# Performance work log

Hardware: AMD Instinct MI355X
Metric: run time of the kernel (lower is better)

## Reference

```python
import jax, jax.numpy as jnp
import numpy as np
import math

T, B, V, D = 8, 32, 50257, 256
N = 4096            # memory slots
H = 4               # attention heads
L = 2               # transformer layers
K = 3               # shift width
HALF = K // 2
WIN = 16            # controller window
RH, WH = 1, 1       # read / write heads
EPS = 1e-12


def _pe(win, d):
    pos = jnp.arange(win, dtype=jnp.float32)[:, None]
    div = jnp.exp(jnp.arange(0, d, 2, dtype=jnp.float32) * (-math.log(10000.0) / d))
    pe = jnp.zeros((win, d), dtype=jnp.float32)
    pe = pe.at[:, 0::2].set(jnp.sin(pos * div))
    pe = pe.at[:, 1::2].set(jnp.cos(pos * div))
    return pe[:, None, :]


def _ln(x, g, b, eps=1e-5):
    mu = x.mean(-1, keepdims=True)
    var = ((x - mu) ** 2).mean(-1, keepdims=True)
    return (x - mu) * jax.lax.rsqrt(var + eps) * g + b


def _mha(x, Wqkv, bqkv, Wo, bo):
    S, Bc, Dm = x.shape
    dh = Dm // H
    qkv = x @ Wqkv.T + bqkv
    q, k, v = jnp.split(qkv, 3, axis=-1)
    q = q.reshape(S, Bc, H, dh)
    k = k.reshape(S, Bc, H, dh)
    v = v.reshape(S, Bc, H, dh)
    logits = jnp.einsum('sbhd,tbhd->bhst', q, k) / math.sqrt(dh)
    a = jax.nn.softmax(logits, axis=-1)
    o = jnp.einsum('bhst,tbhd->sbhd', a, v).reshape(S, Bc, Dm)
    return o @ Wo.T + bo


def _addressing(key_v, beta, gate, shift, gamma, prev_w, memory):
    # key_v [B,M], beta/gate/gamma [B,1], shift [B,K], prev_w [B,N], memory [B,N,M]
    key_n = key_v / (jnp.linalg.norm(key_v, axis=-1, keepdims=True) + EPS)
    mem_n = memory / (jnp.linalg.norm(memory, axis=-1, keepdims=True) + EPS)
    cos = jnp.einsum('bnm,bm->bn', mem_n, key_n)
    wc = jax.nn.softmax(jax.nn.softplus(beta) * cos, axis=-1)
    g = jax.nn.sigmoid(gate)
    wg = g * wc + (1.0 - g) * prev_w
    s = jax.nn.softmax(shift, axis=-1)
    shifted = sum(s[:, k:k + 1] * jnp.roll(wg, k - HALF, axis=-1) for k in range(K))
    gp = 1.0 + jax.nn.softplus(gamma)
    wt = (shifted + EPS) ** gp
    return wt / (wt.sum(-1, keepdims=True) + EPS)


def setup_inputs() -> dict:
    key = jax.random.key(0)
    ks = iter(jax.random.split(key, 40))
    def w(shape, s=0.02):
        return jax.random.normal(next(ks), shape, jnp.float32) * s
    return {
        'tokens': jax.random.randint(next(ks), (T, B), 0, V, jnp.int32),
        'emb_W': w((V, D)),
        'read_gate_W': w((D, D)), 'read_gate_b': jnp.zeros((D,)),
        'film_W': w((2 * D, D)), 'film_b': jnp.zeros((2 * D,)),
        't_Wqkv': w((L, 3 * D, D)), 't_bqkv': jnp.zeros((L, 3 * D)),
        't_Wo': w((L, D, D)), 't_bo': jnp.zeros((L, D)),
        't_ln1_g': jnp.ones((L, D)), 't_ln1_b': jnp.zeros((L, D)),
        't_ln2_g': jnp.ones((L, D)), 't_ln2_b': jnp.zeros((L, D)),
        't_W1': w((L, 4 * D, D)), 't_b1': jnp.zeros((L, 4 * D)),
        't_W2': w((L, D, 4 * D)), 't_b2': jnp.zeros((L, D)),
        'out_ln_g': jnp.ones((D,)), 'out_ln_b': jnp.zeros((D,)),
        'lstm_Wih': w((2, 4 * D, D)), 'lstm_Whh': w((2, 4 * D, D)),
        'lstm_bih': jnp.zeros((2, 4 * D)), 'lstm_bhh': jnp.zeros((2, 4 * D)),
        'head_W': w((V, D)), 'head_b': jnp.zeros((V,)),
        'read_W': w((D + 3 + K, D)), 'read_b': jnp.zeros((D + 3 + K,)),
        'write_W': w((3 * D + 3 + K, D)), 'write_b': jnp.zeros((3 * D + 3 + K,)),
    }


def reference(tokens, emb_W, read_gate_W, read_gate_b, film_W, film_b,
              t_Wqkv, t_bqkv, t_Wo, t_bo, t_ln1_g, t_ln1_b, t_ln2_g, t_ln2_b,
              t_W1, t_b1, t_W2, t_b2, out_ln_g, out_ln_b,
              lstm_Wih, lstm_Whh, lstm_bih, lstm_bhh,
              head_W, head_b, read_W, read_b, write_W, write_b):
    pe = _pe(WIN, D)
    memory = jnp.zeros((B, N, D), jnp.float32)
    read_w = jnp.zeros((B, RH, N), jnp.float32).at[:, :, 0].set(1.0)
    write_w = jnp.zeros((B, WH, N), jnp.float32).at[:, :, 0].set(1.0)
    record = jnp.zeros((B, D), jnp.float32)
    hx = jnp.zeros((2, B, D), jnp.float32)
    cx = jnp.zeros((2, B, D), jnp.float32)
    hist = jnp.zeros((1, B, D), jnp.float32)
    logits_all = []
    for t in range(T):  # T fixed, sequential recurrence (context length grows)
        emb = emb_W[tokens[t]]                               # [B,D]
        r = jnp.einsum('bhn,bnm->bm', read_w, memory)        # sum over read heads
        fp = record @ film_W.T + film_b
        gam = 1.0 + jnp.tanh(fp[:, :D])
        bet = fp[:, D:]
        rg = jax.nn.sigmoid(record @ read_gate_W.T + read_gate_b)
        x_in = gam * emb + bet + rg * r
        ctx = jnp.concatenate([hist, x_in[None]], axis=0)
        if ctx.shape[0] > WIN:
            ctx = ctx[-WIN:]
        hist = ctx
        h = ctx + pe[:ctx.shape[0]]
        for l in range(L):  # norm_first pre-LN encoder layers (eval, relu FFN)
            h = h + _mha(_ln(h, t_ln1_g[l], t_ln1_b[l]), t_Wqkv[l], t_bqkv[l], t_Wo[l], t_bo[l])
            h = h + (jax.nn.relu(_ln(h, t_ln2_g[l], t_ln2_b[l]) @ t_W1[l].T + t_b1[l]) @ t_W2[l].T + t_b2[l])
        c_out = _ln(h[-1], out_ln_g, out_ln_b)
        # 2-layer LSTM single step (torch gate order i,f,g,o)
        x_l = c_out
        new_h, new_c = [], []
        for l in range(2):
            gates = x_l @ lstm_Wih[l].T + lstm_bih[l] + hx[l] @ lstm_Whh[l].T + lstm_bhh[l]
            i_g, f_g, g_g, o_g = jnp.split(gates, 4, axis=-1)
            c_new = jax.nn.sigmoid(f_g) * cx[l] + jax.nn.sigmoid(i_g) * jnp.tanh(g_g)
            h_new = jax.nn.sigmoid(o_g) * jnp.tanh(c_new)
            new_h.append(h_new); new_c.append(c_new)
            x_l = h_new
        hx = jnp.stack(new_h); cx = jnp.stack(new_c)
        record = hx[-1]
        c_out = c_out + x_l
        logits_all.append(c_out @ head_W.T + head_b)
        # read addressing
        rp = (c_out @ read_W.T + read_b).reshape(B, RH, -1)
        new_rw = []
        for hh in range(RH):
            p = rp[:, hh]
            new_rw.append(_addressing(p[:, :D], p[:, D:D + 1], p[:, D + 1:D + 2],
                                      p[:, D + 2:D + 2 + K], p[:, D + 2 + K:D + 3 + K],
                                      read_w[:, hh], memory))
        read_w = jnp.stack(new_rw, axis=1)
        # write addressing + erase/add (addressing uses pre-update memory)
        wp = (c_out @ write_W.T + write_b).reshape(B, WH, -1)
        mem_pre = memory
        new_ww = []
        for hh in range(WH):
            p = wp[:, hh]
            wt = _addressing(p[:, :D], p[:, D:D + 1], p[:, D + 1:D + 2],
                             p[:, D + 2:D + 2 + K], p[:, D + 2 + K:D + 3 + K],
                             write_w[:, hh], mem_pre)
            erase = jax.nn.sigmoid(p[:, D + 3 + K:2 * D + 3 + K])
            add = jnp.tanh(p[:, 2 * D + 3 + K:3 * D + 3 + K])
            memory = memory * (1.0 - wt[:, :, None] * erase[:, None, :]) + wt[:, :, None] * add[:, None, :]
            new_ww.append(wt)
        write_w = jnp.stack(new_ww, axis=1)
    return jnp.stack(logits_all, axis=0)  # [T, B, V]
```

## Files before the change

### kernel.cpp

```cpp
#include <hip/hip_runtime.h>
#include <math.h>

#define TT 8
#define BB 32
#define VV 50257
#define DD 256
#define NN 4096
#define EPS_ 1e-12f

typedef __attribute__((ext_vector_type(8))) short short8;
typedef __attribute__((ext_vector_type(4))) float f32x4;

__device__ __forceinline__ float sigf(float x) { return 1.f / (1.f + expf(-x)); }
__device__ __forceinline__ float softplusf_(float x) { return fmaxf(x, 0.f) + log1pf(expf(-fabsf(x))); }
__device__ __forceinline__ unsigned f2bf(float f) {
  union { float f; unsigned u; } c; c.f = f;
  return (c.u + 0x7FFFu + ((c.u >> 16) & 1u)) >> 16;
}
__device__ __forceinline__ float bf2f(unsigned u16) {
  union { unsigned u; float f; } c; c.u = u16 << 16; return c.f;
}

__device__ __forceinline__ float blk_sum(float v, float* s) {
#pragma unroll
  for (int o = 32; o > 0; o >>= 1) v += __shfl_down(v, o);
  __syncthreads();
  if ((threadIdx.x & 63) == 0) s[threadIdx.x >> 6] = v;
  __syncthreads();
  return s[0] + s[1] + s[2] + s[3];
}
__device__ __forceinline__ float blk_max(float v, float* s) {
#pragma unroll
  for (int o = 32; o > 0; o >>= 1) v = fmaxf(v, __shfl_down(v, o));
  __syncthreads();
  if ((threadIdx.x & 63) == 0) s[threadIdx.x >> 6] = v;
  __syncthreads();
  return fmaxf(fmaxf(s[0], s[1]), fmaxf(s[2], s[3]));
}

__global__ void init_k(float* rw, float* ww, float* hpe) {
  int i = blockIdx.x * 256 + threadIdx.x;
  if (i < BB) { rw[(size_t)i * NN] = 1.f; ww[(size_t)i * NN] = 1.f; }
  if (i < BB * DD) hpe[i] = (i & 1) ? 1.f : 0.f;
}

__global__ void cvtw_k(const float* __restrict__ W, unsigned short* __restrict__ Wh, int n4) {
  int i = blockIdx.x * 256 + threadIdx.x;
  if (i >= n4) return;
  float4 v = *(const float4*)(W + (size_t)i * 4);
  uint2 p;
  p.x = f2bf(v.x) | (f2bf(v.y) << 16);
  p.y = f2bf(v.z) | (f2bf(v.w) << 16);
  *(uint2*)(Wh + (size_t)i * 4) = p;
}

__global__ void catlstm_k(const float* __restrict__ Wih, const float* __restrict__ Whh,
                          const float* __restrict__ bih, const float* __restrict__ bhh,
                          unsigned short* __restrict__ Wc, float* __restrict__ cb) {
  int i = blockIdx.x * 256 + threadIdx.x;
  if (i >= 2 * 1024 * 512) return;
  int k = i & 511, np = (i >> 9) & 1023, l = i >> 19;
  int d = np >> 2, gate = np & 3;
  int src = gate * 256 + d;
  float v = (k < 256) ? Wih[((size_t)l * 1024 + src) * 256 + k]
                      : Whh[((size_t)l * 1024 + src) * 256 + (k - 256)];
  Wc[i] = (unsigned short)f2bf(v);
  if (k == 0) cb[l * 1024 + np] = bih[l * 1024 + src] + bhh[l * 1024 + src];
}

__global__ void catrw_k(const float* __restrict__ rW, const float* __restrict__ rb,
                        const float* __restrict__ wW, const float* __restrict__ wb,
                        unsigned short* __restrict__ Wrw, float* __restrict__ brw) {
  int i = blockIdx.x * 256 + threadIdx.x;
  if (i >= 1036 * 256) return;
  int k = i & 255, n = i >> 8;
  float v = (n < 262) ? rW[(size_t)n * 256 + k] : wW[(size_t)(n - 262) * 256 + k];
  Wrw[i] = (unsigned short)f2bf(v);
  if (k == 0) brw[n] = (n < 262) ? rb[n] : wb[n - 262];
}

__global__ void brc_k(const float* __restrict__ fb, const float* __restrict__ rb, float* __restrict__ brc) {
  int i = blockIdx.x * 256 + threadIdx.x;
  if (i < 512) brc[i] = fb[i];
  else if (i < 768) brc[i] = rb[i - 512];
}

__global__ __launch_bounds__(256) void ln0_k(const float* __restrict__ hpe,
                                             const float* __restrict__ g1, const float* __restrict__ b1,
                                             unsigned short* __restrict__ q1b) {
  __shared__ float s8[8];
  int b = blockIdx.x, d = threadIdx.x;
  float v = hpe[(size_t)b * 256 + d];
  float mu = blk_sum(v, s8) * (1.f / 256.f);
  float dd = v - mu;
  float var = blk_sum(dd * dd, s8) * (1.f / 256.f);
  float rs = rsqrtf(var + 1e-5f);
  q1b[(size_t)b * 256 + d] = (unsigned short)f2bf(dd * rs * g1[d] + b1[d]);
}

template <int EPI>
__global__ __launch_bounds__(256) void gA_k(const unsigned short* __restrict__ A,
                                            const unsigned short* __restrict__ W,
                                            const float* __restrict__ bias,
                                            float* __restrict__ Cf,
                                            unsigned short* __restrict__ Cb,
                                            int ldc, int Nlim) {
  const int tid = threadIdx.x, w = tid >> 6, l = tid & 63, r = l & 15, q = l >> 4;
  const int m0 = blockIdx.y * 32;
  const int n = blockIdx.x * 64 + w * 16 + r;
  const unsigned short* Ap = A + (size_t)m0 * 256;
  const unsigned short* Wp = W + (size_t)n * 256;
  f32x4 acc0 = {0.f, 0.f, 0.f, 0.f}, acc1 = {0.f, 0.f, 0.f, 0.f};
#pragma unroll
  for (int kt = 0; kt < 8; ++kt) {
    short8 a0 = *(const short8*)(Ap + r * 256 + kt * 32 + q * 8);
    short8 a1 = *(const short8*)(Ap + (16 + r) * 256 + kt * 32 + q * 8);
    short8 bf = *(const short8*)(Wp + kt * 32 + q * 8);
    acc0 = __builtin_amdgcn_mfma_f32_16x16x32_bf16(a0, bf, acc0, 0, 0, 0);
    acc1 = __builtin_amdgcn_mfma_f32_16x16x32_bf16(a1, bf, acc1, 0, 0, 0);
  }
  if (n >= Nlim) return;
  float bb = bias[n];
#pragma unroll
  for (int e = 0; e < 4; ++e) {
    int m1 = m0 + q * 4 + e, m2 = m1 + 16;
    float v1 = acc0[e] + bb, v2 = acc1[e] + bb;
    if constexpr (EPI == 0) {
      Cf[(size_t)m1 * ldc + n] = v1;
      Cf[(size_t)m2 * ldc + n] = v2;
    } else {
      Cb[(size_t)m1 * ldc + n] = (unsigned short)f2bf(fmaxf(v1, 0.f));
      Cb[(size_t)m2 * ldc + n] = (unsigned short)f2bf(fmaxf(v2, 0.f));
    }
  }
}

template <int K, int OLN>
__global__ __launch_bounds__(256) void gB_k(const unsigned short* __restrict__ A,
                                            const unsigned short* __restrict__ W,
                                            const float* __restrict__ bias,
                                            const float* __restrict__ resid,
                                            float* __restrict__ Hout,
                                            const float* __restrict__ lng,
                                            const float* __restrict__ lnb,
                                            unsigned short* __restrict__ Xb, int xstride,
                                            float* __restrict__ c_out) {
  __shared__ float hv[32][260];
  const int tid = threadIdx.x, w = tid >> 6, l = tid & 63, r = l & 15, q = l >> 4;
  const int m0 = blockIdx.x * 32;
  const unsigned short* Ap = A + (size_t)m0 * K;
  const unsigned short* Wp0 = W + (size_t)(w * 64 + 0 + r) * K;
  const unsigned short* Wp1 = W + (size_t)(w * 64 + 16 + r) * K;
  const unsigned short* Wp2 = W + (size_t)(w * 64 + 32 + r) * K;
  const unsigned short* Wp3 = W + (size_t)(w * 64 + 48 + r) * K;
  f32x4 acc0[4], acc1[4];
#pragma unroll
  for (int j = 0; j < 4; ++j) { acc0[j] = {0.f, 0.f, 0.f, 0.f}; acc1[j] = {0.f, 0.f, 0.f, 0.f}; }
#pragma unroll 4
  for (int kt = 0; kt < K / 32; ++kt) {
    short8 a0 = *(const short8*)(Ap + (size_t)r * K + kt * 32 + q * 8);
    short8 a1 = *(const short8*)(Ap + (size_t)(16 + r) * K + kt * 32 + q * 8);
    short8 b0 = *(const short8*)(Wp0 + kt * 32 + q * 8);
    short8 b1 = *(const short8*)(Wp1 + kt * 32 + q * 8);
    short8 b2 = *(const short8*)(Wp2 + kt * 32 + q * 8);
    short8 b3 = *(const short8*)(Wp3 + kt * 32 + q * 8);
    acc0[0] = __builtin_amdgcn_mfma_f32_16x16x32_bf16(a0, b0, acc0[0], 0, 0, 0);
    acc1[0] = __builtin_amdgcn_mfma_f32_16x16x32_bf16(a1, b0, acc1[0], 0, 0, 0);
    acc0[1] = __builtin_amdgcn_mfma_f32_16x16x32_bf16(a0, b1, acc0[1], 0, 0, 0);
    acc1[1] = __builtin_amdgcn_mfma_f32_16x16x32_bf16(a1, b1, acc1[1], 0, 0, 0);
    acc0[2] = __builtin_amdgcn_mfma_f32_16x16x32_bf16(a0, b2, acc0[2], 0, 0, 0);
    acc1[2] = __builtin_amdgcn_mfma_f32_16x16x32_bf16(a1, b2, acc1[2], 0, 0, 0);
    acc0[3] = __builtin_amdgcn_mfma_f32_16x16x32_bf16(a0, b3, acc0[3], 0, 0, 0);
    acc1[3] = __builtin_amdgcn_mfma_f32_16x16x32_bf16(a1, b3, acc1[3], 0, 0, 0);
  }
#pragma unroll
  for (int j = 0; j < 4; ++j) {
    int n = w * 64 + j * 16 + r;
    float bb = bias[n];
#pragma unroll
    for (int e = 0; e < 4; ++e) {
      int m1 = q * 4 + e, m2 = m1 + 16;
      float v1 = acc0[j][e] + bb + resid[(size_t)(m0 + m1) * 256 + n];
      float v2 = acc1[j][e] + bb + resid[(size_t)(m0 + m2) * 256 + n];
      Hout[(size_t)(m0 + m1) * 256 + n] = v1;
      Hout[(size_t)(m0 + m2) * 256 + n] = v2;
      hv[m1][n] = v1;
      hv[m2][n] = v2;
    }
  }
  __syncthreads();
  const float4 g4 = *(const float4*)(lng + l * 4);
  const float4 be4 = *(const float4*)(lnb + l * 4);
#pragma unroll
  for (int i = 0; i < 8; ++i) {
    int row = w * 8 + i;
    float4 v = *(const float4*)&hv[row][l * 4];
    float s1 = v.x + v.y + v.z + v.w;
    float s2 = v.x * v.x + v.y * v.y + v.z * v.z + v.w * v.w;
#pragma unroll
    for (int o = 32; o > 0; o >>= 1) { s1 += __shfl_xor(s1, o); s2 += __shfl_xor(s2, o); }
    float mu = s1 * (1.f / 256.f);
    float var = fmaxf(s2 * (1.f / 256.f) - mu * mu, 0.f);
    float rs = rsqrtf(var + 1e-5f);
    float y0 = (v.x - mu) * rs * g4.x + be4.x;
    float y1 = (v.y - mu) * rs * g4.y + be4.y;
    float y2 = (v.z - mu) * rs * g4.z + be4.z;
    float y3 = (v.w - mu) * rs * g4.w + be4.w;
    uint2 pk;
    pk.x = f2bf(y0) | (f2bf(y1) << 16);
    pk.y = f2bf(y2) | (f2bf(y3) << 16);
    *(uint2*)(Xb + (size_t)(m0 + row) * xstride + l * 4) = pk;
    if constexpr (OLN) {
      float4 cv = make_float4(y0, y1, y2, y3);
      *(float4*)(c_out + (size_t)(m0 + row) * 256 + l * 4) = cv;
    }
  }
}

template <int LAST>
__global__ __launch_bounds__(256) void gL_k(const unsigned short* __restrict__ A,
                                            const unsigned short* __restrict__ W,
                                            const float* __restrict__ cbias,
                                            float* __restrict__ cx,
                                            unsigned short* __restrict__ li_own,
                                            unsigned short* __restrict__ li_next,
                                            const float* __restrict__ c_outp,
                                            unsigned short* __restrict__ cfinb,
                                            unsigned short* __restrict__ record_b) {
  __shared__ float g[32][68];
  const int tid = threadIdx.x, w = tid >> 6, l = tid & 63, r = l & 15, q = l >> 4;
  const int n = blockIdx.x * 64 + w * 16 + r;
  const unsigned short* Wp = W + (size_t)n * 512;
  f32x4 acc0 = {0.f, 0.f, 0.f, 0.f}, acc1 = {0.f, 0.f, 0.f, 0.f};
#pragma unroll 4
  for (int kt = 0; kt < 16; ++kt) {
    short8 a0 = *(const short8*)(A + (size_t)r * 512 + kt * 32 + q * 8);
    short8 a1 = *(const short8*)(A + (size_t)(16 + r) * 512 + kt * 32 + q * 8);
    short8 bf = *(const short8*)(Wp + kt * 32 + q * 8);
    acc0 = __builtin_amdgcn_mfma_f32_16x16x32_bf16(a0, bf, acc0, 0, 0, 0);
    acc1 = __builtin_amdgcn_mfma_f32_16x16x32_bf16(a1, bf, acc1, 0, 0, 0);
  }
  float bb = cbias[n];
  int nb = w * 16 + r;
#pragma unroll
  for (int e = 0; e < 4; ++e) {
    g[q * 4 + e][nb] = acc0[e] + bb;
    g[16 + q * 4 + e][nb] = acc1[e] + bb;
  }
  __syncthreads();
#pragma unroll
  for (int h2 = 0; h2 < 2; ++h2) {
    int u = tid + 256 * h2;
    int b = u >> 4, dd = u & 15;
    int dg = blockIdx.x * 16 + dd;
    float gi = g[b][dd * 4 + 0], gf = g[b][dd * 4 + 1];
    float gg = g[b][dd * 4 + 2], go = g[b][dd * 4 + 3];
    float c = sigf(gf) * cx[b * 256 + dg] + sigf(gi) * tanhf(gg);
    float hN = sigf(go) * tanhf(c);
    cx[b * 256 + dg] = c;
    li_own[(size_t)b * 512 + 256 + dg] = (unsigned short)f2bf(hN);
    if constexpr (LAST) {
      record_b[b * 256 + dg] = (unsigned short)f2bf(hN);
      cfinb[b * 256 + dg] = (unsigned short)f2bf(c_outp[b * 256 + dg] + hN);
    } else {
      li_next[(size_t)b * 512 + dg] = (unsigned short)f2bf(hN);
    }
  }
}

__global__ __launch_bounds__(256) void xinpw_k(const int* __restrict__ tokens,
                                               const float* __restrict__ embW,
                                               const float* __restrict__ fp,
                                               const float* __restrict__ rvec,
                                               const float* __restrict__ g1, const float* __restrict__ b1,
                                               float* __restrict__ hpe,
                                               unsigned short* __restrict__ q1b, int t) {
  __shared__ float s8[8];
  int b = blockIdx.x, d = threadIdx.x;
  float gam = 1.f + tanhf(fp[(size_t)b * 768 + d]);
  float bet = fp[(size_t)b * 768 + 256 + d];
  float rg = sigf(fp[(size_t)b * 768 + 512 + d]);
  int tok = tokens[t * BB + b];
  float emb = embW[(size_t)tok * 256 + d];
  float ang = (float)(t + 1) * expf(-logf(10000.f) * (float)(d & ~1) / 256.f);
  float pe = (d & 1) ? cosf(ang) : sinf(ang);
  float x = gam * emb + bet + rg * rvec[b * 256 + d] + pe;
  hpe[((size_t)(t + 1) * BB + b) * 256 + d] = x;
  float mu = blk_sum(x, s8) * (1.f / 256.f);
  float dd = x - mu;
  float var = blk_sum(dd * dd, s8) * (1.f / 256.f);
  float rs = rsqrtf(var + 1e-5f);
  q1b[((size_t)(t + 1) * BB + b) * 256 + d] = (unsigned short)f2bf(dd * rs * g1[d] + b1[d]);
}

__global__ __launch_bounds__(128) void attn_k(const float* __restrict__ qkv,
                                              unsigned short* __restrict__ ao, int S) {
  int bh = blockIdx.x;
  int b = bh >> 2, h = bh & 3;
  __shared__ float q[9][64], k[9][64], v[9][64], lg[9][12];
  int tid = threadIdx.x;
  for (int i = tid; i < S * 64; i += 128) {
    int s = i >> 6, d = i & 63;
    const float* base = qkv + (size_t)(s * BB + b) * 768 + h * 64 + d;
    q[s][d] = base[0]; k[s][d] = base[256]; v[s][d] = base[512];
  }
  __syncthreads();
  for (int p = tid; p < S * S; p += 128) {
    int s = p / S, t2 = p % S;
    float acc = 0.f;
    for (int d = 0; d < 64; ++d) acc += q[s][d] * k[t2][d];
    lg[s][t2] = acc * 0.125f;
  }
  __syncthreads();
  if (tid < S) {
    float mx = -1e30f;
    for (int t2 = 0; t2 < S; ++t2) mx = fmaxf(mx, lg[tid][t2]);
    float sum = 0.f;
    for (int t2 = 0; t2 < S; ++t2) { float e = expf(lg[tid][t2] - mx); lg[tid][t2] = e; sum += e; }
    float inv = 1.f / sum;
    for (int t2 = 0; t2 < S; ++t2) lg[tid][t2] *= inv;
  }
  __syncthreads();
  for (int i = tid; i < S * 64; i += 128) {
    int s = i >> 6, d = i & 63;
    float o = 0.f;
    for (int t2 = 0; t2 < S; ++t2) o += lg[s][t2] * v[t2][d];
    ao[(size_t)(s * BB + b) * 256 + h * 64 + d] = (unsigned short)f2bf(o);
  }
}

__global__ __launch_bounds__(64) void attnl_k(const float* __restrict__ qkv,
                                              unsigned short* __restrict__ ao, int S) {
  int bh = blockIdx.x;
  int b = bh >> 2, h = bh & 3;
  int d = threadIdx.x;
  __shared__ float sc[9];
  float qd = qkv[(size_t)((S - 1) * BB + b) * 768 + h * 64 + d];
  for (int j = 0; j < S; ++j) {
    float p = qd * qkv[(size_t)(j * BB + b) * 768 + h * 64 + 256 + d];
#pragma unroll
    for (int o = 32; o > 0; o >>= 1) p += __shfl_down(p, o);
    if (d == 0) sc[j] = p * 0.125f;
  }
  __syncthreads();
  float mx = -1e30f;
  for (int j = 0; j < S; ++j) mx = fmaxf(mx, sc[j]);
  float pj[9], sum = 0.f;
  for (int j = 0; j < S; ++j) { pj[j] = expf(sc[j] - mx); sum += pj[j]; }
  float inv = 1.f / sum;
  float o = 0.f;
  for (int j = 0; j < S; ++j) o += pj[j] * inv * qkv[(size_t)(j * BB + b) * 768 + h * 64 + 512 + d];
  ao[(size_t)b * 256 + h * 64 + d] = (unsigned short)f2bf(o);
}

__global__ __launch_bounds__(256) void head_k(const unsigned short* __restrict__ Wh,
                                              const unsigned short* __restrict__ Ah,
                                              const float* __restrict__ hb,
                                              float* __restrict__ out) {
  const int tid = threadIdx.x;
  const int w = tid >> 6, l = tid & 63;
  const int r = l & 15, q = l >> 4;
  const int n = blockIdx.x * 64 + w * 16 + r;
  const int nc = n < VV ? n : VV - 1;
  const short* Ap = (const short*)Ah;
  const short* Wp = (const short*)Wh + (size_t)nc * 256;
  short8 a0[8], a1[8], bf[8];
#pragma unroll
  for (int kt = 0; kt < 8; ++kt) {
    a0[kt] = *(const short8*)(Ap + r * 256 + kt * 32 + q * 8);
    a1[kt] = *(const short8*)(Ap + (16 + r) * 256 + kt * 32 + q * 8);
    bf[kt] = *(const short8*)(Wp + kt * 32 + q * 8);
  }
  f32x4 acc0 = {0.f, 0.f, 0.f, 0.f}, acc1 = {0.f, 0.f, 0.f, 0.f};
#pragma unroll
  for (int kt = 0; kt < 8; ++kt) {
    acc0 = __builtin_amdgcn_mfma_f32_16x16x32_bf16(a0[kt], bf[kt], acc0, 0, 0, 0);
    acc1 = __builtin_amdgcn_mfma_f32_16x16x32_bf16(a1[kt], bf[kt], acc1, 0, 0, 0);
  }
  if (n < VV) {
    float bb = hb[n];
#pragma unroll
    for (int e = 0; e < 4; ++e) {
      int m = q * 4 + e;
      out[(size_t)m * VV + n] = acc0[e] + bb;
      out[(size_t)(16 + m) * VV + n] = acc1[e] + bb;
    }
  }
}

__global__ __launch_bounds__(256) void passA_k(const unsigned short* __restrict__ mem,
                                               const float* __restrict__ rpwp,
                                               float* __restrict__ dr,
                                               float* __restrict__ dw,
                                               float* __restrict__ nrm) {
  __shared__ float kr[256], kw[256];
  int b = blockIdx.y, tid = threadIdx.x;
  kr[tid] = rpwp[(size_t)b * 1036 + tid];
  kw[tid] = rpwp[(size_t)b * 1036 + 262 + tid];
  __syncthreads();
  int w = tid >> 6, lane = tid & 63;
  float4 kr4 = *(float4*)&kr[lane * 4];
  float4 kw4 = *(float4*)&kw[lane * 4];
  int n0 = blockIdx.x * 16 + w * 4;
  for (int rr = 0; rr < 4; ++rr) {
    int n = n0 + rr;
    const unsigned short* row = mem + ((size_t)b * NN + n) * 256;
    uint2 p = *(const uint2*)(row + lane * 4);
    float m0 = bf2f(p.x & 0xffffu), m1 = bf2f(p.x >> 16);
    float m2 = bf2f(p.y & 0xffffu), m3 = bf2f(p.y >> 16);
    float pr = m0 * kr4.x + m1 * kr4.y + m2 * kr4.z + m3 * kr4.w;
    float pw = m0 * kw4.x + m1 * kw4.y + m2 * kw4.z + m3 * kw4.w;
    float pn = m0 * m0 + m1 * m1 + m2 * m2 + m3 * m3;
#pragma unroll
    for (int o = 32; o > 0; o >>= 1) {
      pr += __shfl_down(pr, o); pw += __shfl_down(pw, o); pn += __shfl_down(pn, o);
    }
    if (lane == 0) {
      dr[(size_t)b * NN + n] = pr;
      dw[(size_t)b * NN + n] = pw;
      nrm[(size_t)b * NN + n] = pn;
    }
  }
}

__global__ __launch_bounds__(256) void addr_k(const float* __restrict__ dr,
                                              const float* __restrict__ dw,
                                              const float* __restrict__ nrm,
                                              const float* __restrict__ rpwp,
                                              float* rw, float* ww,
                                              float* __restrict__ ea,
                                              float* __restrict__ rvec) {
  __shared__ float wg[4096];
  __shared__ float s8[8];
  int head = blockIdx.x & 1, b = blockIdx.x >> 1;
  int tid = threadIdx.x;
  const float* p = rpwp + (size_t)b * 1036 + (head ? 262 : 0);
  const float* dot = (head ? dw : dr) + (size_t)b * NN;
  const float* n2 = nrm + (size_t)b * NN;
  float* wout = (head ? ww : rw) + (size_t)b * NN;

  float kv = p[tid];
  float kn = sqrtf(blk_sum(kv * kv, s8)) + EPS_;
  float beta = p[256], gate = p[257], sh0 = p[258], sh1 = p[259], sh2 = p[260], gamma = p[261];
  float spb = softplusf_(beta);
  float g = sigf(gate);
  float mx3 = fmaxf(sh0, fmaxf(sh1, sh2));
  float e0 = expf(sh0 - mx3), e1 = expf(sh1 - mx3), e2 = expf(sh2 - mx3);
  float esum = e0 + e1 + e2;
  float s0 = e0 / esum, s1 = e1 / esum, s2 = e2 / esum;
  float gp = 1.f + softplusf_(gamma);

  float l[16];
  float lmax = -1e30f;
#pragma unroll
  for (int i = 0; i < 16; ++i) {
    int n = tid + i * 256;
    float cs = dot[n] / ((sqrtf(n2[n]) + EPS_) * kn);
    l[i] = spb * cs;
    lmax = fmaxf(lmax, l[i]);
  }
  float Mx = blk_max(lmax, s8);
  float es = 0.f;
#pragma unroll
  for (int i = 0; i < 16; ++i) { l[i] = expf(l[i] - Mx); es += l[i]; }
  float SS = blk_sum(es, s8);
  float inv = 1.f / SS;
#pragma unroll
  for (int i = 0; i < 16; ++i) {
    int n = tid + i * 256;
    wg[n] = g * l[i] * inv + (1.f - g) * wout[n];
  }
  __syncthreads();
  float wt[16];
  float wsum = 0.f;
#pragma unroll
  for (int i = 0; i < 16; ++i) {
    int n = tid + i * 256;
    float sh = s0 * wg[(n + 1) & 4095] + s1 * wg[n] + s2 * wg[(n + 4095) & 4095];
    wt[i] = powf(sh + EPS_, gp);
    wsum += wt[i];
  }
  float WS = blk_sum(wsum, s8) + EPS_;
  float winv = 1.f / WS;
#pragma unroll
  for (int i = 0; i < 16; ++i) wout[tid + i * 256] = wt[i] * winv;

  if (head) {
    ea[(size_t)b * 512 + tid] = sigf(p[262 + tid]);
    ea[(size_t)b * 512 + 256 + tid] = tanhf(p[518 + tid]);
  } else {
    rvec[(size_t)b * 256 + tid] = 0.f;
  }
}

template <int FIRST>
__global__ __launch_bounds__(256) void passB_k(unsigned short* mem, const float* __restrict__ ww,
                                               const float* __restrict__ rw,
                                               const float* __restrict__ ea,
                                               float* __restrict__ rvec) {
  __shared__ float eS[256], aS[256];
  __shared__ float rred[4][256];
  int b = blockIdx.y, tid = threadIdx.x;
  eS[tid] = ea[(size_t)b * 512 + tid];
  aS[tid] = ea[(size_t)b * 512 + 256 + tid];
  __syncthreads();
  int w = tid >> 6, lane = tid & 63;
  float4 e4 = *(float4*)&eS[lane * 4];
  float4 a4 = *(float4*)&aS[lane * 4];
  float4 racc = make_float4(0.f, 0.f, 0.f, 0.f);
  int n0 = blockIdx.x * 128 + w * 32;
  for (int rr = 0; rr < 32; ++rr) {
    int n = n0 + rr;
    float wt = ww[(size_t)b * NN + n];
    float rwv = rw[(size_t)b * NN + n];
    unsigned short* row = mem + ((size_t)b * NN + n) * 256;
    float m0, m1, m2, m3;
    if (FIRST) {
      m0 = wt * a4.x; m1 = wt * a4.y; m2 = wt * a4.z; m3 = wt * a4.w;
    } else {
      uint2 p = *(const uint2*)(row + lane * 4);
      m0 = bf2f(p.x & 0xffffu) * (1.f - wt * e4.x) + wt * a4.x;
      m1 = bf2f(p.x >> 16) * (1.f - wt * e4.y) + wt * a4.y;
      m2 = bf2f(p.y & 0xffffu) * (1.f - wt * e4.z) + wt * a4.z;
      m3 = bf2f(p.y >> 16) * (1.f - wt * e4.w) + wt * a4.w;
    }
    uint2 pk;
    pk.x = f2bf(m0) | (f2bf(m1) << 16);
    pk.y = f2bf(m2) | (f2bf(m3) << 16);
    *(uint2*)(row + lane * 4) = pk;
    racc.x += rwv * m0; racc.y += rwv * m1; racc.z += rwv * m2; racc.w += rwv * m3;
  }
  rred[w][lane * 4 + 0] = racc.x;
  rred[w][lane * 4 + 1] = racc.y;
  rred[w][lane * 4 + 2] = racc.z;
  rred[w][lane * 4 + 3] = racc.w;
  __syncthreads();
  float s = rred[0][tid] + rred[1][tid] + rred[2][tid] + rred[3][tid];
  atomicAdd(rvec + (size_t)b * 256 + tid, s);
}

extern "C" void kernel_launch(void* const* d_in, const int* in_sizes, int n_in,
                              void* d_out, int out_size, void* d_ws, size_t ws_size,
                              hipStream_t stream) {
  const int* tokens = (const int*)d_in[0];
  const float* emb_W = (const float*)d_in[1];
  const float* read_gate_W = (const float*)d_in[2];
  const float* read_gate_b = (const float*)d_in[3];
  const float* film_W = (const float*)d_in[4];
  const float* film_b = (const float*)d_in[5];
  const float* t_Wqkv = (const float*)d_in[6];
  const float* t_bqkv = (const float*)d_in[7];
  const float* t_Wo = (const float*)d_in[8];
  const float* t_bo = (const float*)d_in[9];
  const float* t_ln1_g = (const float*)d_in[10];
  const float* t_ln1_b = (const float*)d_in[11];
  const float* t_ln2_g = (const float*)d_in[12];
  const float* t_ln2_b = (const float*)d_in[13];
  const float* t_W1 = (const float*)d_in[14];
  const float* t_b1 = (const float*)d_in[15];
  const float* t_W2 = (const float*)d_in[16];
  const float* t_b2 = (const float*)d_in[17];
  const float* out_ln_g = (const float*)d_in[18];
  const float* out_ln_b = (const float*)d_in[19];
  const float* lstm_Wih = (const float*)d_in[20];
  const float* lstm_Whh = (const float*)d_in[21];
  const float* lstm_bih = (const float*)d_in[22];
  const float* lstm_bhh = (const float*)d_in[23];
  const float* head_W = (const float*)d_in[24];
  const float* head_b = (const float*)d_in[25];
  const float* read_W = (const float*)d_in[26];
  const float* read_b = (const float*)d_in[27];
  const float* write_W = (const float*)d_in[28];
  const float* write_b = (const float*)d_in[29];
  float* out = (float*)d_out;

  float* ws = (float*)d_ws;
  size_t off = 0;
  float* read_w = ws + off; off += (size_t)BB * NN;
  float* write_w = ws + off; off += (size_t)BB * NN;
  float* cx = ws + off; off += 2 * BB * DD;
  float* r_vec = ws + off; off += BB * DD;
  float* dot_r = ws + off; off += (size_t)BB * NN;
  float* dot_w = ws + off; off += (size_t)BB * NN;
  float* norm2 = ws + off; off += (size_t)BB * NN;
  unsigned short* record_b = (unsigned short*)(ws + off); off += BB * DD / 2;
  unsigned short* lstm_in_b = (unsigned short*)(ws + off); off += 2 * BB * 512 / 2;
  size_t zero_floats = off;
  unsigned short* memory = (unsigned short*)(ws + off); off += (size_t)BB * NN * DD / 2;
  float* hpe = ws + off; off += 9 * BB * DD;
  float* h = ws + off; off += 9 * BB * DD;
  float* h2 = ws + off; off += BB * DD;
  float* qkvC = ws + off; off += 9 * BB * 768;
  float* qkv2 = ws + off; off += 9 * BB * 768;
  float* fp = ws + off; off += BB * 768;
  float* c_out = ws + off; off += BB * DD;
  float* rpwp = ws + off; off += BB * 1036;
  float* ea = ws + off; off += BB * 2 * DD;
  unsigned short* q1b = (unsigned short*)(ws + off); off += 9 * BB * DD / 2;
  unsigned short* q2b = (unsigned short*)(ws + off); off += 9 * BB * DD / 2;
  unsigned short* x2b = (unsigned short*)(ws + off); off += 9 * BB * DD / 2;
  unsigned short* x2b2 = (unsigned short*)(ws + off); off += BB * DD / 2;
  unsigned short* ao_b = (unsigned short*)(ws + off); off += 9 * BB * DD / 2;
  unsigned short* ao2_b = (unsigned short*)(ws + off); off += BB * DD / 2;
  unsigned short* mid_b = (unsigned short*)(ws + off); off += 9 * BB * 1024 / 2;
  unsigned short* cfinb = (unsigned short*)(ws + off); off += BB * DD / 2;
  unsigned short* Wh = (unsigned short*)(ws + off); off += (size_t)VV * 256 / 2;
  unsigned short* Wq_b = (unsigned short*)(ws + off); off += 2 * 768 * 256 / 2;
  unsigned short* Wo_b = (unsigned short*)(ws + off); off += 2 * 256 * 256 / 2;
  unsigned short* W1_b = (unsigned short*)(ws + off); off += 2 * 1024 * 256 / 2;
  unsigned short* W2_b = (unsigned short*)(ws + off); off += 2 * 256 * 1024 / 2;
  unsigned short* Wc_b = (unsigned short*)(ws + off); off += 2 * 1024 * 512 / 2;
  unsigned short* Wrw_b = (unsigned short*)(ws + off); off += 1088 * 256 / 2;
  unsigned short* FR_b = (unsigned short*)(ws + off); off += 768 * 256 / 2;
  float* cb2 = ws + off; off += 2 * 1024;
  float* brw = ws + off; off += 1040;
  float* brc = ws + off; off += 768;
  if (ws_size < off * sizeof(float)) return;

  (void)hipMemsetAsync(ws, 0, zero_floats * sizeof(float), stream);
  (void)hipMemsetAsync(Wrw_b + (size_t)1036 * 256, 0, (size_t)52 * 256 * 2, stream);
  init_k<<<32, 256, 0, stream>>>(read_w, write_w, hpe);
  cvtw_k<<<(VV * 256 / 4 + 255) / 256, 256, 0, stream>>>(head_W, Wh, VV * 256 / 4);
  cvtw_k<<<(2 * 768 * 256 / 4 + 255) / 256, 256, 0, stream>>>(t_Wqkv, Wq_b, 2 * 768 * 256 / 4);
  cvtw_k<<<(2 * 256 * 256 / 4 + 255) / 256, 256, 0, stream>>>(t_Wo, Wo_b, 2 * 256 * 256 / 4);
  cvtw_k<<<(2 * 1024 * 256 / 4 + 255) / 256, 256, 0, stream>>>(t_W1, W1_b, 2 * 1024 * 256 / 4);
  cvtw_k<<<(2 * 256 * 1024 / 4 + 255) / 256, 256, 0, stream>>>(t_W2, W2_b, 2 * 256 * 1024 / 4);
  cvtw_k<<<(512 * 256 / 4 + 255) / 256, 256, 0, stream>>>(film_W, FR_b, 512 * 256 / 4);
  cvtw_k<<<(256 * 256 / 4 + 255) / 256, 256, 0, stream>>>(read_gate_W, FR_b + 512 * 256, 256 * 256 / 4);
  catlstm_k<<<4096, 256, 0, stream>>>(lstm_Wih, lstm_Whh, lstm_bih, lstm_bhh, Wc_b, cb2);
  catrw_k<<<1036, 256, 0, stream>>>(read_W, read_b, write_W, write_b, Wrw_b, brw);
  brc_k<<<3, 256, 0, stream>>>(film_b, read_gate_b, brc);
  ln0_k<<<BB, 256, 0, stream>>>(hpe, t_ln1_g, t_ln1_b, q1b);
  gA_k<0><<<dim3(12, 1), 256, 0, stream>>>(q1b, Wq_b, t_bqkv, qkvC, nullptr, 768, 768);

  for (int t = 0; t < TT; ++t) {
    const int S = t + 2;

    gA_k<0><<<dim3(12, 1), 256, 0, stream>>>(record_b, FR_b, brc, fp, nullptr, 768, 768);
    xinpw_k<<<BB, 256, 0, stream>>>(tokens, emb_W, fp, r_vec, t_ln1_g, t_ln1_b, hpe, q1b, t);
    gA_k<0><<<dim3(12, 1), 256, 0, stream>>>(q1b + (size_t)(t + 1) * BB * 256, Wq_b, t_bqkv,
                                             qkvC + (size_t)(t + 1) * BB * 768, nullptr, 768, 768);
    attn_k<<<BB * 4, 128, 0, stream>>>(qkvC, ao_b, S);
    gB_k<256, 0><<<S, 256, 0, stream>>>(ao_b, Wo_b, t_bo, hpe, h, t_ln2_g, t_ln2_b, x2b, 256, nullptr);
    gA_k<1><<<dim3(16, S), 256, 0, stream>>>(x2b, W1_b, t_b1, nullptr, mid_b, 1024, 1024);
    gB_k<1024, 0><<<S, 256, 0, stream>>>(mid_b, W2_b, t_b2, h, h, t_ln1_g + 256, t_ln1_b + 256, q2b, 256, nullptr);

    gA_k<0><<<dim3(12, S), 256, 0, stream>>>(q2b, Wq_b + 768 * 256, t_bqkv + 768, qkv2, nullptr, 768, 768);
    attnl_k<<<BB * 4, 64, 0, stream>>>(qkv2, ao2_b, S);
    gB_k<256, 0><<<1, 256, 0, stream>>>(ao2_b, Wo_b + 256 * 256, t_bo + 256, h + (size_t)(S - 1) * BB * 256,
                                        h2, t_ln2_g + 256, t_ln2_b + 256, x2b2, 256, nullptr);
    gA_k<1><<<dim3(16, 1), 256, 0, stream>>>(x2b2, W1_b + 1024 * 256, t_b1 + 1024, nullptr, mid_b, 1024, 1024);
    gB_k<1024, 1><<<1, 256, 0, stream>>>(mid_b, W2_b + 256 * 1024, t_b2 + 256, h2, h2,
                                         out_ln_g, out_ln_b, lstm_in_b, 512, c_out);

    gL_k<0><<<16, 256, 0, stream>>>(lstm_in_b, Wc_b, cb2, cx, lstm_in_b, lstm_in_b + BB * 512,
                                    nullptr, nullptr, nullptr);
    gL_k<1><<<16, 256, 0, stream>>>(lstm_in_b + BB * 512, Wc_b + (size_t)1024 * 512, cb2 + 1024,
                                    cx + BB * DD, lstm_in_b + BB * 512, nullptr, c_out, cfinb, record_b);

    head_k<<<(VV + 63) / 64, 256, 0, stream>>>(Wh, cfinb, head_b, out + (size_t)t * BB * VV);

    if (t < TT - 1) {
      gA_k<0><<<dim3(17, 1), 256, 0, stream>>>(cfinb, Wrw_b, brw, rpwp, nullptr, 1036, 1036);
      if (t > 0)
        passA_k<<<dim3(NN / 16, BB), 256, 0, stream>>>(memory, rpwp, dot_r, dot_w, norm2);
      addr_k<<<2 * BB, 256, 0, stream>>>(dot_r, dot_w, norm2, rpwp, read_w, write_w, ea, r_vec);
      if (t == 0)
        passB_k<1><<<dim3(NN / 128, BB), 256, 0, stream>>>(memory, write_w, read_w, ea, r_vec);
      else
        passB_k<0><<<dim3(NN / 128, BB), 256, 0, stream>>>(memory, write_w, read_w, ea, r_vec);
    }
  }
}
```

Before: 1.679 ms.

## Fuse per-step controller kernels into persistent kernel with grid barrier

```diff
diff --git a/kernel.cpp b/kernel.cpp
--- a/kernel.cpp
+++ b/kernel.cpp
@@ -6,6 +6,7 @@
 #define VV 50257
 #define DD 256
 #define NN 4096
+#define NB 144
 #define EPS_ 1e-12f
 
 typedef __attribute__((ext_vector_type(8))) short short8;
@@ -36,6 +37,24 @@
   if ((threadIdx.x & 63) == 0) s[threadIdx.x >> 6] = v;
   __syncthreads();
   return fmaxf(fmaxf(s[0], s[1]), fmaxf(s[2], s[3]));
+}
+
+__device__ __forceinline__ void gbar(unsigned* cnt, unsigned* gen) {
+  __syncthreads();
+  if (threadIdx.x == 0) {
+    __threadfence();
+    unsigned g = __hip_atomic_load(gen, __ATOMIC_RELAXED, __HIP_MEMORY_SCOPE_AGENT);
+    unsigned a = __hip_atomic_fetch_add(cnt, 1u, __ATOMIC_ACQ_REL, __HIP_MEMORY_SCOPE_AGENT);
+    if (a == NB - 1) {
+      __hip_atomic_store(cnt, 0u, __ATOMIC_RELAXED, __HIP_MEMORY_SCOPE_AGENT);
+      __hip_atomic_fetch_add(gen, 1u, __ATOMIC_RELEASE, __HIP_MEMORY_SCOPE_AGENT);
+    } else {
+      while (__hip_atomic_load(gen, __ATOMIC_ACQUIRE, __HIP_MEMORY_SCOPE_AGENT) == g)
+        __builtin_amdgcn_s_sleep(2);
+    }
+    __threadfence();
+  }
+  __syncthreads();
 }
 
 __global__ void init_k(float* rw, float* ww, float* hpe) {
@@ -98,23 +117,18 @@
   q1b[(size_t)b * 256 + d] = (unsigned short)f2bf(dd * rs * g1[d] + b1[d]);
 }
 
-template <int EPI>
-__global__ __launch_bounds__(256) void gA_k(const unsigned short* __restrict__ A,
-                                            const unsigned short* __restrict__ W,
-                                            const float* __restrict__ bias,
-                                            float* __restrict__ Cf,
-                                            unsigned short* __restrict__ Cb,
-                                            int ldc, int Nlim) {
+__device__ __forceinline__ void gA32f_dev(const unsigned short* __restrict__ A,
+                                          const unsigned short* __restrict__ W,
+                                          const float* __restrict__ bias,
+                                          float* __restrict__ Cf, int ldc, int Nlim, int nblk) {
   const int tid = threadIdx.x, w = tid >> 6, l = tid & 63, r = l & 15, q = l >> 4;
-  const int m0 = blockIdx.y * 32;
-  const int n = blockIdx.x * 64 + w * 16 + r;
-  const unsigned short* Ap = A + (size_t)m0 * 256;
+  const int n = nblk * 64 + w * 16 + r;
   const unsigned short* Wp = W + (size_t)n * 256;
   f32x4 acc0 = {0.f, 0.f, 0.f, 0.f}, acc1 = {0.f, 0.f, 0.f, 0.f};
 #pragma unroll
   for (int kt = 0; kt < 8; ++kt) {
-    short8 a0 = *(const short8*)(Ap + r * 256 + kt * 32 + q * 8);
-    short8 a1 = *(const short8*)(Ap + (16 + r) * 256 + kt * 32 + q * 8);
+    short8 a0 = *(const short8*)(A + r * 256 + kt * 32 + q * 8);
+    short8 a1 = *(const short8*)(A + (16 + r) * 256 + kt * 32 + q * 8);
     short8 bf = *(const short8*)(Wp + kt * 32 + q * 8);
     acc0 = __builtin_amdgcn_mfma_f32_16x16x32_bf16(a0, bf, acc0, 0, 0, 0);
     acc1 = __builtin_amdgcn_mfma_f32_16x16x32_bf16(a1, bf, acc1, 0, 0, 0);
@@ -123,32 +137,49 @@
   float bb = bias[n];
 #pragma unroll
   for (int e = 0; e < 4; ++e) {
-    int m1 = m0 + q * 4 + e, m2 = m1 + 16;
-    float v1 = acc0[e] + bb, v2 = acc1[e] + bb;
-    if constexpr (EPI == 0) {
-      Cf[(size_t)m1 * ldc + n] = v1;
-      Cf[(size_t)m2 * ldc + n] = v2;
-    } else {
-      Cb[(size_t)m1 * ldc + n] = (unsigned short)f2bf(fmaxf(v1, 0.f));
-      Cb[(size_t)m2 * ldc + n] = (unsigned short)f2bf(fmaxf(v2, 0.f));
-    }
+    int m1 = q * 4 + e, m2 = m1 + 16;
+    Cf[(size_t)m1 * ldc + n] = acc0[e] + bb;
+    Cf[(size_t)m2 * ldc + n] = acc1[e] + bb;
+  }
+}
+
+__device__ __forceinline__ void gA32r_dev(const unsigned short* __restrict__ A,
+                                          const unsigned short* __restrict__ W,
+                                          const float* __restrict__ bias,
+                                          unsigned short* __restrict__ Cb, int ldc, int nblk) {
+  const int tid = threadIdx.x, w = tid >> 6, l = tid & 63, r = l & 15, q = l >> 4;
+  const int n = nblk * 64 + w * 16 + r;
+  const unsigned short* Wp = W + (size_t)n * 256;
+  f32x4 acc0 = {0.f, 0.f, 0.f, 0.f}, acc1 = {0.f, 0.f, 0.f, 0.f};
+#pragma unroll
+  for (int kt = 0; kt < 8; ++kt) {
+    short8 a0 = *(const short8*)(A + r * 256 + kt * 32 + q * 8);
+    short8 a1 = *(const short8*)(A + (16 + r) * 256 + kt * 32 + q * 8);
+    short8 bf = *(const short8*)(Wp + kt * 32 + q * 8);
+    acc0 = __builtin_amdgcn_mfma_f32_16x16x32_bf16(a0, bf, acc0, 0, 0, 0);
+    acc1 = __builtin_amdgcn_mfma_f32_16x16x32_bf16(a1, bf, acc1, 0, 0, 0);
+  }
+  float bb = bias[n];
+#pragma unroll
+  for (int e = 0; e < 4; ++e) {
+    int m1 = q * 4 + e, m2 = m1 + 16;
+    Cb[(size_t)m1 * ldc + n] = (unsigned short)f2bf(fmaxf(acc0[e] + bb, 0.f));
+    Cb[(size_t)m2 * ldc + n] = (unsigned short)f2bf(fmaxf(acc1[e] + bb, 0.f));
   }
 }
 
 template <int K, int OLN>
-__global__ __launch_bounds__(256) void gB_k(const unsigned short* __restrict__ A,
-                                            const unsigned short* __restrict__ W,
-                                            const float* __restrict__ bias,
-                                            const float* __restrict__ resid,
-                                            float* __restrict__ Hout,
-                                            const float* __restrict__ lng,
-                                            const float* __restrict__ lnb,
-                                            unsigned short* __restrict__ Xb, int xstride,
-                                            float* __restrict__ c_out) {
-  __shared__ float hv[32][260];
+__device__ __forceinline__ void gB_dev(const unsigned short* __restrict__ A,
+                                       const unsigned short* __restrict__ W,
+                                       const float* __restrict__ bias,
+                                       const float* __restrict__ resid,
+                                       float* __restrict__ Hout,
+                                       const float* __restrict__ lng,
+                                       const float* __restrict__ lnb,
+                                       unsigned short* __restrict__ Xb, int xstride,
+                                       float* __restrict__ c_out, float* smemf) {
+  float (*hv)[260] = (float(*)[260])smemf;
   const int tid = threadIdx.x, w = tid >> 6, l = tid & 63, r = l & 15, q = l >> 4;
-  const int m0 = blockIdx.x * 32;
-  const unsigned short* Ap = A + (size_t)m0 * K;
   const unsigned short* Wp0 = W + (size_t)(w * 64 + 0 + r) * K;
   const unsigned short* Wp1 = W + (size_t)(w * 64 + 16 + r) * K;
   const unsigned short* Wp2 = W + (size_t)(w * 64 + 32 + r) * K;
@@ -158,8 +189,8 @@
   for (int j = 0; j < 4; ++j) { acc0[j] = {0.f, 0.f, 0.f, 0.f}; acc1[j] = {0.f, 0.f, 0.f, 0.f}; }
 #pragma unroll 4
   for (int kt = 0; kt < K / 32; ++kt) {
-    short8 a0 = *(const short8*)(Ap + (size_t)r * K + kt * 32 + q * 8);
-    short8 a1 = *(const short8*)(Ap + (size_t)(16 + r) * K + kt * 32 + q * 8);
+    short8 a0 = *(const short8*)(A + (size_t)r * K + kt * 32 + q * 8);
+    short8 a1 = *(const short8*)(A + (size_t)(16 + r) * K + kt * 32 + q * 8);
     short8 b0 = *(const short8*)(Wp0 + kt * 32 + q * 8);
     short8 b1 = *(const short8*)(Wp1 + kt * 32 + q * 8);
     short8 b2 = *(const short8*)(Wp2 + kt * 32 + q * 8);
@@ -180,10 +211,10 @@
 #pragma unroll
     for (int e = 0; e < 4; ++e) {
       int m1 = q * 4 + e, m2 = m1 + 16;
-      float v1 = acc0[j][e] + bb + resid[(size_t)(m0 + m1) * 256 + n];
-      float v2 = acc1[j][e] + bb + resid[(size_t)(m0 + m2) * 256 + n];
-      Hout[(size_t)(m0 + m1) * 256 + n] = v1;
-      Hout[(size_t)(m0 + m2) * 256 + n] = v2;
+      float v1 = acc0[j][e] + bb + resid[(size_t)m1 * 256 + n];
+      float v2 = acc1[j][e] + bb + resid[(size_t)m2 * 256 + n];
+      Hout[(size_t)m1 * 256 + n] = v1;
+      Hout[(size_t)m2 * 256 + n] = v2;
       hv[m1][n] = v1;
       hv[m2][n] = v2;
     }
@@ -209,27 +240,29 @@
     uint2 pk;
     pk.x = f2bf(y0) | (f2bf(y1) << 16);
     pk.y = f2bf(y2) | (f2bf(y3) << 16);
-    *(uint2*)(Xb + (size_t)(m0 + row) * xstride + l * 4) = pk;
+    *(uint2*)(Xb + (size_t)row * xstride + l * 4) = pk;
     if constexpr (OLN) {
       float4 cv = make_float4(y0, y1, y2, y3);
-      *(float4*)(c_out + (size_t)(m0 + row) * 256 + l * 4) = cv;
-    }
-  }
+      *(float4*)(c_out + (size_t)row * 256 + l * 4) = cv;
+    }
+  }
+  __syncthreads();
 }
 
 template <int LAST>
-__global__ __launch_bounds__(256) void gL_k(const unsigned short* __restrict__ A,
-                                            const unsigned short* __restrict__ W,
-                                            const float* __restrict__ cbias,
-                                            float* __restrict__ cx,
-                                            unsigned short* __restrict__ li_own,
-                                            unsigned short* __restrict__ li_next,
-                                            const float* __restrict__ c_outp,
-                                            unsigned short* __restrict__ cfinb,
-                                            unsigned short* __restrict__ record_b) {
-  __shared__ float g[32][68];
+__device__ __forceinline__ void gL_dev(const unsigned short* __restrict__ A,
+                                       const unsigned short* __restrict__ W,
+                                       const float* __restrict__ cbias,
+                                       float* __restrict__ cx,
+                                       unsigned short* __restrict__ li_own,
+                                       unsigned short* __restrict__ li_next,
+                                       const float* __restrict__ c_outp,
+                                       unsigned short* __restrict__ cfinb,
+                                       unsigned short* __restrict__ record_b,
+                                       int nblk, float* smemf) {
+  float (*g)[68] = (float(*)[68])smemf;
   const int tid = threadIdx.x, w = tid >> 6, l = tid & 63, r = l & 15, q = l >> 4;
-  const int n = blockIdx.x * 64 + w * 16 + r;
+  const int n = nblk * 64 + w * 16 + r;
   const unsigned short* Wp = W + (size_t)n * 512;
   f32x4 acc0 = {0.f, 0.f, 0.f, 0.f}, acc1 = {0.f, 0.f, 0.f, 0.f};
 #pragma unroll 4
@@ -252,7 +285,7 @@
   for (int h2 = 0; h2 < 2; ++h2) {
     int u = tid + 256 * h2;
     int b = u >> 4, dd = u & 15;
-    int dg = blockIdx.x * 16 + dd;
+    int dg = nblk * 16 + dd;
     float gi = g[b][dd * 4 + 0], gf = g[b][dd * 4 + 1];
     float gg = g[b][dd * 4 + 2], go = g[b][dd * 4 + 3];
     float c = sigf(gf) * cx[b * 256 + dg] + sigf(gi) * tanhf(gg);
@@ -266,148 +299,244 @@
       li_next[(size_t)b * 512 + dg] = (unsigned short)f2bf(hN);
     }
   }
-}
-
-__global__ __launch_bounds__(256) void xinpw_k(const int* __restrict__ tokens,
-                                               const float* __restrict__ embW,
-                                               const float* __restrict__ fp,
-                                               const float* __restrict__ rvec,
-                                               const float* __restrict__ g1, const float* __restrict__ b1,
-                                               float* __restrict__ hpe,
-                                               unsigned short* __restrict__ q1b, int t) {
-  __shared__ float s8[8];
-  int b = blockIdx.x, d = threadIdx.x;
-  float gam = 1.f + tanhf(fp[(size_t)b * 768 + d]);
-  float bet = fp[(size_t)b * 768 + 256 + d];
-  float rg = sigf(fp[(size_t)b * 768 + 512 + d]);
-  int tok = tokens[t * BB + b];
-  float emb = embW[(size_t)tok * 256 + d];
-  float ang = (float)(t + 1) * expf(-logf(10000.f) * (float)(d & ~1) / 256.f);
-  float pe = (d & 1) ? cosf(ang) : sinf(ang);
-  float x = gam * emb + bet + rg * rvec[b * 256 + d] + pe;
-  hpe[((size_t)(t + 1) * BB + b) * 256 + d] = x;
-  float mu = blk_sum(x, s8) * (1.f / 256.f);
-  float dd = x - mu;
-  float var = blk_sum(dd * dd, s8) * (1.f / 256.f);
-  float rs = rsqrtf(var + 1e-5f);
-  q1b[((size_t)(t + 1) * BB + b) * 256 + d] = (unsigned short)f2bf(dd * rs * g1[d] + b1[d]);
-}
-
-__global__ __launch_bounds__(128) void attn_k(const float* __restrict__ qkv,
-                                              unsigned short* __restrict__ ao, int S) {
-  int bh = blockIdx.x;
-  int b = bh >> 2, h = bh & 3;
-  __shared__ float q[9][64], k[9][64], v[9][64], lg[9][12];
+  __syncthreads();
+}
+
+__device__ __forceinline__ void attn1_dev(const float* __restrict__ qkv,
+                                          unsigned short* __restrict__ ao,
+                                          int S, int b, int h, float* smemf) {
+  float* q = smemf;
+  float* k = q + 9 * 64;
+  float* v = k + 9 * 64;
+  float* lg = v + 9 * 64;
   int tid = threadIdx.x;
-  for (int i = tid; i < S * 64; i += 128) {
+  for (int i = tid; i < S * 64; i += 256) {
     int s = i >> 6, d = i & 63;
     const float* base = qkv + (size_t)(s * BB + b) * 768 + h * 64 + d;
-    q[s][d] = base[0]; k[s][d] = base[256]; v[s][d] = base[512];
-  }
-  __syncthreads();
-  for (int p = tid; p < S * S; p += 128) {
+    q[s * 64 + d] = base[0]; k[s * 64 + d] = base[256]; v[s * 64 + d] = base[512];
+  }
+  __syncthreads();
+  for (int p = tid; p < S * S; p += 256) {
     int s = p / S, t2 = p % S;
     float acc = 0.f;
-    for (int d = 0; d < 64; ++d) acc += q[s][d] * k[t2][d];
-    lg[s][t2] = acc * 0.125f;
+    for (int d = 0; d < 64; ++d) acc += q[s * 64 + d] * k[t2 * 64 + d];
+    lg[s * 12 + t2] = acc * 0.125f;
   }
   __syncthreads();
   if (tid < S) {
     float mx = -1e30f;
-    for (int t2 = 0; t2 < S; ++t2) mx = fmaxf(mx, lg[tid][t2]);
+    for (int t2 = 0; t2 < S; ++t2) mx = fmaxf(mx, lg[tid * 12 + t2]);
     float sum = 0.f;
-    for (int t2 = 0; t2 < S; ++t2) { float e = expf(lg[tid][t2] - mx); lg[tid][t2] = e; sum += e; }
+    for (int t2 = 0; t2 < S; ++t2) { float e = expf(lg[tid * 12 + t2] - mx); lg[tid * 12 + t2] = e; sum += e; }
     float inv = 1.f / sum;
-    for (int t2 = 0; t2 < S; ++t2) lg[tid][t2] *= inv;
-  }
-  __syncthreads();
-  for (int i = tid; i < S * 64; i += 128) {
+    for (int t2 = 0; t2 < S; ++t2) lg[tid * 12 + t2] *= inv;
+  }
+  __syncthreads();
+  for (int i = tid; i < S * 64; i += 256) {
     int s = i >> 6, d = i & 63;
     float o = 0.f;
-    for (int t2 = 0; t2 < S; ++t2) o += lg[s][t2] * v[t2][d];
+    for (int t2 = 0; t2 < S; ++t2) o += lg[s * 12 + t2] * v[t2 * 64 + d];
     ao[(size_t)(s * BB + b) * 256 + h * 64 + d] = (unsigned short)f2bf(o);
   }
-}
-
-__global__ __launch_bounds__(64) void attnl_k(const float* __restrict__ qkv,
-                                              unsigned short* __restrict__ ao, int S) {
-  int bh = blockIdx.x;
-  int b = bh >> 2, h = bh & 3;
-  int d = threadIdx.x;
-  __shared__ float sc[9];
+  __syncthreads();
+}
+
+__device__ __forceinline__ void attnl_dev(const float* __restrict__ qkv,
+                                          unsigned short* __restrict__ ao,
+                                          int S, int b, float* smemf) {
+  float* sc = smemf;
+  int h = threadIdx.x >> 6, d = threadIdx.x & 63;
   float qd = qkv[(size_t)((S - 1) * BB + b) * 768 + h * 64 + d];
   for (int j = 0; j < S; ++j) {
     float p = qd * qkv[(size_t)(j * BB + b) * 768 + h * 64 + 256 + d];
 #pragma unroll
     for (int o = 32; o > 0; o >>= 1) p += __shfl_down(p, o);
-    if (d == 0) sc[j] = p * 0.125f;
+    if (d == 0) sc[h * 9 + j] = p * 0.125f;
   }
   __syncthreads();
   float mx = -1e30f;
-  for (int j = 0; j < S; ++j) mx = fmaxf(mx, sc[j]);
+  for (int j = 0; j < S; ++j) mx = fmaxf(mx, sc[h * 9 + j]);
   float pj[9], sum = 0.f;
-  for (int j = 0; j < S; ++j) { pj[j] = expf(sc[j] - mx); sum += pj[j]; }
+  for (int j = 0; j < S; ++j) { pj[j] = expf(sc[h * 9 + j] - mx); sum += pj[j]; }
   float inv = 1.f / sum;
   float o = 0.f;
   for (int j = 0; j < S; ++j) o += pj[j] * inv * qkv[(size_t)(j * BB + b) * 768 + h * 64 + 512 + d];
   ao[(size_t)b * 256 + h * 64 + d] = (unsigned short)f2bf(o);
-}
-
-__global__ __launch_bounds__(256) void head_k(const unsigned short* __restrict__ Wh,
-                                              const unsigned short* __restrict__ Ah,
-                                              const float* __restrict__ hb,
-                                              float* __restrict__ out) {
+  __syncthreads();
+}
+
+struct SP {
+  const int* tokens; const float* embW;
+  float* fp; float* r_vec;
+  const float* ln1g0; const float* ln1b0;
+  float* hpe; unsigned short* q1b;
+  const unsigned short* Wq0; const unsigned short* Wq1;
+  const float* bq0; const float* bq1;
+  float* qkvC; float* qkv2;
+  unsigned short* ao1; unsigned short* ao2;
+  const unsigned short* Wo0; const unsigned short* Wo1;
+  const float* bo0; const float* bo1;
+  float* h; float* h2;
+  const float* ln2g0; const float* ln2b0; const float* ln2g1; const float* ln2b1;
+  const float* ln1g1; const float* ln1b1;
+  unsigned short* x2b; unsigned short* x2b2; unsigned short* q2b;
+  const unsigned short* W10; const unsigned short* W11;
+  const float* b10; const float* b11;
+  unsigned short* mid_b;
+  const unsigned short* W20; const unsigned short* W21;
+  const float* b20; const float* b21;
+  const float* olng; const float* olnb;
+  unsigned short* lstm_in; float* c_out;
+  const unsigned short* Wc0; const unsigned short* Wc1;
+  const float* cb0; const float* cb1;
+  float* cx0; float* cx1;
+  unsigned short* cfinb; unsigned short* record_b;
+  const unsigned short* Wrw; const float* brw; float* rpwp;
+  const unsigned short* FRw; const float* brc;
+  unsigned* bar_cnt; unsigned* bar_gen;
+};
+
+__global__ __launch_bounds__(256, 1) void step_k(SP p, int t, int do_aux) {
+  __shared__ float smemf[32 * 260];
+  const int bid = blockIdx.x;
+  const int S = t + 2;
+  unsigned* cnt = p.bar_cnt; unsigned* gen = p.bar_gen;
+
+  if (bid < 32) {
+    int b = bid, d = threadIdx.x;
+    float gam = 1.f + tanhf(p.fp[(size_t)b * 768 + d]);
+    float bet = p.fp[(size_t)b * 768 + 256 + d];
+    float rg = sigf(p.fp[(size_t)b * 768 + 512 + d]);
+    int tok = p.tokens[t * BB + b];
+    float emb = p.embW[(size_t)tok * 256 + d];
+    float ang = (float)(t + 1) * expf(-logf(10000.f) * (float)(d & ~1) / 256.f);
+    float pe = (d & 1) ? cosf(ang) : sinf(ang);
+    float x = gam * emb + bet + rg * p.r_vec[b * 256 + d] + pe;
+    p.hpe[((size_t)(t + 1) * BB + b) * 256 + d] = x;
+    float mu = blk_sum(x, smemf) * (1.f / 256.f);
+    float dd = x - mu;
+    float var = blk_sum(dd * dd, smemf) * (1.f / 256.f);
+    float rs = rsqrtf(var + 1e-5f);
+    p.q1b[((size_t)(t + 1) * BB + b) * 256 + d] = (unsigned short)f2bf(dd * rs * p.ln1g0[d] + p.ln1b0[d]);
+  }
+  gbar(cnt, gen);
+  if (bid < 12)
+    gA32f_dev(p.q1b + (size_t)(t + 1) * BB * 256, p.Wq0, p.bq0,
+              p.qkvC + (size_t)(t + 1) * BB * 768, 768, 768, bid);
+  gbar(cnt, gen);
+  if (bid < 128) attn1_dev(p.qkvC, p.ao1, S, bid >> 2, bid & 3, smemf);
+  gbar(cnt, gen);
+  if (bid < S)
+    gB_dev<256, 0>(p.ao1 + (size_t)bid * 32 * 256, p.Wo0, p.bo0,
+                   p.hpe + (size_t)bid * 32 * 256, p.h + (size_t)bid * 32 * 256,
+                   p.ln2g0, p.ln2b0, p.x2b + (size_t)bid * 32 * 256, 256, nullptr, smemf);
+  gbar(cnt, gen);
+  if (bid < S * 16) {
+    int s = bid >> 4, nt = bid & 15;
+    gA32r_dev(p.x2b + (size_t)s * 32 * 256, p.W10, p.b10, p.mid_b + (size_t)s * 32 * 1024, 1024, nt);
+  }
+  gbar(cnt, gen);
+  if (bid < S)
+    gB_dev<1024, 0>(p.mid_b + (size_t)bid * 32 * 1024, p.W20, p.b20,
+                    p.h + (size_t)bid * 32 * 256, p.h + (size_t)bid * 32 * 256,
+                    p.ln1g1, p.ln1b1, p.q2b + (size_t)bid * 32 * 256, 256, nullptr, smemf);
+  gbar(cnt, gen);
+  if (bid < S * 12) {
+    int s = bid / 12, nt = bid % 12;
+    gA32f_dev(p.q2b + (size_t)s * 32 * 256, p.Wq1, p.bq1, p.qkv2 + (size_t)s * BB * 768, 768, 768, nt);
+  }
+  gbar(cnt, gen);
+  if (bid < 32) attnl_dev(p.qkv2, p.ao2, S, bid, smemf);
+  gbar(cnt, gen);
+  if (bid == 0)
+    gB_dev<256, 0>(p.ao2, p.Wo1, p.bo1, p.h + (size_t)(S - 1) * 32 * 256, p.h2,
+                   p.ln2g1, p.ln2b1, p.x2b2, 256, nullptr, smemf);
+  gbar(cnt, gen);
+  if (bid < 16) gA32r_dev(p.x2b2, p.W11, p.b11, p.mid_b, 1024, bid);
+  gbar(cnt, gen);
+  if (bid == 0)
+    gB_dev<1024, 1>(p.mid_b, p.W21, p.b21, p.h2, p.h2, p.olng, p.olnb, p.lstm_in, 512, p.c_out, smemf);
+  gbar(cnt, gen);
+  if (bid < 16)
+    gL_dev<0>(p.lstm_in, p.Wc0, p.cb0, p.cx0, p.lstm_in, p.lstm_in + BB * 512,
+              nullptr, nullptr, nullptr, bid, smemf);
+  gbar(cnt, gen);
+  if (bid < 16)
+    gL_dev<1>(p.lstm_in + BB * 512, p.Wc1, p.cb1, p.cx1, p.lstm_in + BB * 512, nullptr,
+              p.c_out, p.cfinb, p.record_b, bid, smemf);
+  gbar(cnt, gen);
+  if (do_aux) {
+    if (bid < 17) gA32f_dev(p.cfinb, p.Wrw, p.brw, p.rpwp, 1036, 1036, bid);
+    else if (bid < 29) gA32f_dev(p.record_b, p.FRw, p.brc, p.fp, 768, 768, bid - 17);
+  }
+}
+
+__global__ __launch_bounds__(256) void gA_k(const unsigned short* __restrict__ A,
+                                            const unsigned short* __restrict__ W,
+                                            const float* __restrict__ bias,
+                                            float* __restrict__ Cf, int ldc, int Nlim) {
+  gA32f_dev(A, W, bias, Cf, ldc, Nlim, blockIdx.x);
+}
+
+__global__ __launch_bounds__(256) void fusePA_k(const unsigned short* __restrict__ Wh,
+                                                const unsigned short* __restrict__ Ah,
+                                                const float* __restrict__ hb,
+                                                float* __restrict__ out,
+                                                const unsigned short* __restrict__ mem,
+                                                const float* __restrict__ rpwp,
+                                                float* __restrict__ dr,
+                                                float* __restrict__ dw,
+                                                float* __restrict__ nrm, int pa_on) {
+  __shared__ float kr[256], kw[256];
+  const int bid = blockIdx.x;
   const int tid = threadIdx.x;
-  const int w = tid >> 6, l = tid & 63;
-  const int r = l & 15, q = l >> 4;
-  const int n = blockIdx.x * 64 + w * 16 + r;
-  const int nc = n < VV ? n : VV - 1;
-  const short* Ap = (const short*)Ah;
-  const short* Wp = (const short*)Wh + (size_t)nc * 256;
-  short8 a0[8], a1[8], bf[8];
-#pragma unroll
-  for (int kt = 0; kt < 8; ++kt) {
-    a0[kt] = *(const short8*)(Ap + r * 256 + kt * 32 + q * 8);
-    a1[kt] = *(const short8*)(Ap + (16 + r) * 256 + kt * 32 + q * 8);
-    bf[kt] = *(const short8*)(Wp + kt * 32 + q * 8);
-  }
-  f32x4 acc0 = {0.f, 0.f, 0.f, 0.f}, acc1 = {0.f, 0.f, 0.f, 0.f};
-#pragma unroll
-  for (int kt = 0; kt < 8; ++kt) {
-    acc0 = __builtin_amdgcn_mfma_f32_16x16x32_bf16(a0[kt], bf[kt], acc0, 0, 0, 0);
-    acc1 = __builtin_amdgcn_mfma_f32_16x16x32_bf16(a1[kt], bf[kt], acc1, 0, 0, 0);
-  }
-  if (n < VV) {
-    float bb = hb[n];
-#pragma unroll
-    for (int e = 0; e < 4; ++e) {
-      int m = q * 4 + e;
-      out[(size_t)m * VV + n] = acc0[e] + bb;
-      out[(size_t)(16 + m) * VV + n] = acc1[e] + bb;
-    }
-  }
-}
-
-__global__ __launch_bounds__(256) void passA_k(const unsigned short* __restrict__ mem,
-                                               const float* __restrict__ rpwp,
-                                               float* __restrict__ dr,
-                                               float* __restrict__ dw,
-                                               float* __restrict__ nrm) {
-  __shared__ float kr[256], kw[256];
-  int b = blockIdx.y, tid = threadIdx.x;
-  kr[tid] = rpwp[(size_t)b * 1036 + tid];
-  kw[tid] = rpwp[(size_t)b * 1036 + 262 + tid];
+  if (bid < 786) {
+    const int w = tid >> 6, l = tid & 63;
+    const int r = l & 15, q = l >> 4;
+    const int n = bid * 64 + w * 16 + r;
+    const int nc = n < VV ? n : VV - 1;
+    const short* Ap = (const short*)Ah;
+    const short* Wp = (const short*)Wh + (size_t)nc * 256;
+    short8 a0[8], a1[8], bf[8];
+#pragma unroll
+    for (int kt = 0; kt < 8; ++kt) {
+      a0[kt] = *(const short8*)(Ap + r * 256 + kt * 32 + q * 8);
+      a1[kt] = *(const short8*)(Ap + (16 + r) * 256 + kt * 32 + q * 8);
+      bf[kt] = *(const short8*)(Wp + kt * 32 + q * 8);
+    }
+    f32x4 acc0 = {0.f, 0.f, 0.f, 0.f}, acc1 = {0.f, 0.f, 0.f, 0.f};
+#pragma unroll
+    for (int kt = 0; kt < 8; ++kt) {
+      acc0 = __builtin_amdgcn_mfma_f32_16x16x32_bf16(a0[kt], bf[kt], acc0, 0, 0, 0);
+      acc1 = __builtin_amdgcn_mfma_f32_16x16x32_bf16(a1[kt], bf[kt], acc1, 0, 0, 0);
+    }
+    if (n < VV) {
+      float bb = hb[n];
+#pragma unroll
+      for (int e = 0; e < 4; ++e) {
+        int m = q * 4 + e;
+        out[(size_t)m * VV + n] = acc0[e] + bb;
+        out[(size_t)(16 + m) * VV + n] = acc1[e] + bb;
+      }
+    }
+    return;
+  }
+  if (!pa_on) return;
+  const int idx = bid - 786;
+  const int bx = idx & 255, by = idx >> 8;
+  kr[tid] = rpwp[(size_t)by * 1036 + tid];
+  kw[tid] = rpwp[(size_t)by * 1036 + 262 + tid];
   __syncthreads();
   int w = tid >> 6, lane = tid & 63;
   float4 kr4 = *(float4*)&kr[lane * 4];
   float4 kw4 = *(float4*)&kw[lane * 4];
-  int n0 = blockIdx.x * 16 + w * 4;
+  int n0 = bx * 16 + w * 4;
   for (int rr = 0; rr < 4; ++rr) {
     int n = n0 + rr;
-    const unsigned short* row = mem + ((size_t)b * NN + n) * 256;
-    uint2 p = *(const uint2*)(row + lane * 4);
-    float m0 = bf2f(p.x & 0xffffu), m1 = bf2f(p.x >> 16);
-    float m2 = bf2f(p.y & 0xffffu), m3 = bf2f(p.y >> 16);
+    const unsigned short* row = mem + ((size_t)by * NN + n) * 256;
+    uint2 pck = *(const uint2*)(row + lane * 4);
+    float m0 = bf2f(pck.x & 0xffffu), m1 = bf2f(pck.x >> 16);
+    float m2 = bf2f(pck.y & 0xffffu), m3 = bf2f(pck.y >> 16);
     float pr = m0 * kr4.x + m1 * kr4.y + m2 * kr4.z + m3 * kr4.w;
     float pw = m0 * kw4.x + m1 * kw4.y + m2 * kw4.z + m3 * kw4.w;
     float pn = m0 * m0 + m1 * m1 + m2 * m2 + m3 * m3;
@@ -416,9 +545,9 @@
       pr += __shfl_down(pr, o); pw += __shfl_down(pw, o); pn += __shfl_down(pn, o);
     }
     if (lane == 0) {
-      dr[(size_t)b * NN + n] = pr;
-      dw[(size_t)b * NN + n] = pw;
-      nrm[(size_t)b * NN + n] = pn;
+      dr[(size_t)by * NN + n] = pr;
+      dw[(size_t)by * NN + n] = pw;
+      nrm[(size_t)by * NN + n] = pn;
     }
   }
 }
@@ -576,6 +705,7 @@
 
   float* ws = (float*)d_ws;
   size_t off = 0;
+  unsigned* bar = (unsigned*)(ws + off); off += 64;
   float* read_w = ws + off; off += (size_t)BB * NN;
   float* write_w = ws + off; off += (size_t)BB * NN;
   float* cx = ws + off; off += 2 * BB * DD;
@@ -600,7 +730,7 @@
   unsigned short* q2b = (unsigned short*)(ws + off); off += 9 * BB * DD / 2;
   unsigned short* x2b = (unsigned short*)(ws + off); off += 9 * BB * DD / 2;
   unsigned short* x2b2 = (unsigned short*)(ws + off); off += BB * DD / 2;
-  unsigned short* ao_b = (unsigned short*)(ws + off); off += 9 * BB * DD / 2;
+  unsigned short* ao1_b = (unsigned short*)(ws + off); off += 9 * BB * DD / 2;
   unsigned short* ao2_b = (unsigned short*)(ws + off); off += BB * DD / 2;
   unsigned short* mid_b = (unsigned short*)(ws + off); off += 9 * BB * 1024 / 2;
   unsigned short* cfinb = (unsigned short*)(ws + off); off += BB * DD / 2;
@@ -631,39 +761,46 @@
   catrw_k<<<1036, 256, 0, stream>>>(read_W, read_b, write_W, write_b, Wrw_b, brw);
   brc_k<<<3, 256, 0, stream>>>(film_b, read_gate_b, brc);
   ln0_k<<<BB, 256, 0, stream>>>(hpe, t_ln1_g, t_ln1_b, q1b);
-  gA_k<0><<<dim3(12, 1), 256, 0, stream>>>(q1b, Wq_b, t_bqkv, qkvC, nullptr, 768, 768);
+  gA_k<<<12, 256, 0, stream>>>(q1b, Wq_b, t_bqkv, qkvC, 768, 768);
+  gA_k<<<12, 256, 0, stream>>>(record_b, FR_b, brc, fp, 768, 768);
+
+  SP sp;
+  sp.tokens = tokens; sp.embW = emb_W;
+  sp.fp = fp; sp.r_vec = r_vec;
+  sp.ln1g0 = t_ln1_g; sp.ln1b0 = t_ln1_b;
+  sp.hpe = hpe; sp.q1b = q1b;
+  sp.Wq0 = Wq_b; sp.Wq1 = Wq_b + 768 * 256;
+  sp.bq0 = t_bqkv; sp.bq1 = t_bqkv + 768;
+  sp.qkvC = qkvC; sp.qkv2 = qkv2;
+  sp.ao1 = ao1_b; sp.ao2 = ao2_b;
+  sp.Wo0 = Wo_b; sp.Wo1 = Wo_b + 256 * 256;
+  sp.bo0 = t_bo; sp.bo1 = t_bo + 256;
+  sp.h = h; sp.h2 = h2;
+  sp.ln2g0 = t_ln2_g; sp.ln2b0 = t_ln2_b;
+  sp.ln2g1 = t_ln2_g + 256; sp.ln2b1 = t_ln2_b + 256;
+  sp.ln1g1 = t_ln1_g + 256; sp.ln1b1 = t_ln1_b + 256;
+  sp.x2b = x2b; sp.x2b2 = x2b2; sp.q2b = q2b;
+  sp.W10 = W1_b; sp.W11 = W1_b + 1024 * 256;
+  sp.b10 = t_b1; sp.b11 = t_b1 + 1024;
+  sp.mid_b = mid_b;
+  sp.W20 = W2_b; sp.W21 = W2_b + 256 * 1024;
+  sp.b20 = t_b2; sp.b21 = t_b2 + 256;
+  sp.olng = out_ln_g; sp.olnb = out_ln_b;
+  sp.lstm_in = lstm_in_b; sp.c_out = c_out;
+  sp.Wc0 = Wc_b; sp.Wc1 = Wc_b + (size_t)1024 * 512;
+  sp.cb0 = cb2; sp.cb1 = cb2 + 1024;
+  sp.cx0 = cx; sp.cx1 = cx + BB * DD;
+  sp.cfinb = cfinb; sp.record_b = record_b;
+  sp.Wrw = Wrw_b; sp.brw = brw; sp.rpwp = rpwp;
+  sp.FRw = FR_b; sp.brc = brc;
+  sp.bar_cnt = bar; sp.bar_gen = bar + 32;
 
   for (int t = 0; t < TT; ++t) {
-    const int S = t + 2;
-
-    gA_k<0><<<dim3(12, 1), 256, 0, stream>>>(record_b, FR_b, brc, fp, nullptr, 768, 768);
-    xinpw_k<<<BB, 256, 0, stream>>>(tokens, emb_W, fp, r_vec, t_ln1_g, t_ln1_b, hpe, q1b, t);
-    gA_k<0><<<dim3(12, 1), 256, 0, stream>>>(q1b + (size_t)(t + 1) * BB * 256, Wq_b, t_bqkv,
-                                             qkvC + (size_t)(t + 1) * BB * 768, nullptr, 768, 768);
-    attn_k<<<BB * 4, 128, 0, stream>>>(qkvC, ao_b, S);
-    gB_k<256, 0><<<S, 256, 0, stream>>>(ao_b, Wo_b, t_bo, hpe, h, t_ln2_g, t_ln2_b, x2b, 256, nullptr);
-    gA_k<1><<<dim3(16, S), 256, 0, stream>>>(x2b, W1_b, t_b1, nullptr, mid_b, 1024, 1024);
-    gB_k<1024, 0><<<S, 256, 0, stream>>>(mid_b, W2_b, t_b2, h, h, t_ln1_g + 256, t_ln1_b + 256, q2b, 256, nullptr);
-
-    gA_k<0><<<dim3(12, S), 256, 0, stream>>>(q2b, Wq_b + 768 * 256, t_bqkv + 768, qkv2, nullptr, 768, 768);
-    attnl_k<<<BB * 4, 64, 0, stream>>>(qkv2, ao2_b, S);
-    gB_k<256, 0><<<1, 256, 0, stream>>>(ao2_b, Wo_b + 256 * 256, t_bo + 256, h + (size_t)(S - 1) * BB * 256,
-                                        h2, t_ln2_g + 256, t_ln2_b + 256, x2b2, 256, nullptr);
-    gA_k<1><<<dim3(16, 1), 256, 0, stream>>>(x2b2, W1_b + 1024 * 256, t_b1 + 1024, nullptr, mid_b, 1024, 1024);
-    gB_k<1024, 1><<<1, 256, 0, stream>>>(mid_b, W2_b + 256 * 1024, t_b2 + 256, h2, h2,
-                                         out_ln_g, out_ln_b, lstm_in_b, 512, c_out);
-
-    gL_k<0><<<16, 256, 0, stream>>>(lstm_in_b, Wc_b, cb2, cx, lstm_in_b, lstm_in_b + BB * 512,
-                                    nullptr, nullptr, nullptr);
-    gL_k<1><<<16, 256, 0, stream>>>(lstm_in_b + BB * 512, Wc_b + (size_t)1024 * 512, cb2 + 1024,
-                                    cx + BB * DD, lstm_in_b + BB * 512, nullptr, c_out, cfinb, record_b);
-
-    head_k<<<(VV + 63) / 64, 256, 0, stream>>>(Wh, cfinb, head_b, out + (size_t)t * BB * VV);
-
+    step_k<<<NB, 256, 0, stream>>>(sp, t, t < TT - 1);
+    fusePA_k<<<786 + 8192, 256, 0, stream>>>(Wh, cfinb, head_b, out + (size_t)t * BB * VV,
+                                             memory, rpwp, dot_r, dot_w, norm2,
+                                             (t > 0 && t < TT - 1));
     if (t < TT - 1) {
-      gA_k<0><<<dim3(17, 1), 256, 0, stream>>>(cfinb, Wrw_b, brw, rpwp, nullptr, 1036, 1036);
-      if (t > 0)
-        passA_k<<<dim3(NN / 16, BB), 256, 0, stream>>>(memory, rpwp, dot_r, dot_w, norm2);
       addr_k<<<2 * BB, 256, 0, stream>>>(dot_r, dot_w, norm2, rpwp, read_w, write_w, ea, r_vec);
       if (t == 0)
         passB_k<1><<<dim3(NN / 128, BB), 256, 0, stream>>>(memory, write_w, read_w, ea, r_vec);
```

After: 3.415 ms. 2.03x slower.
